# Kernel tuning notes

Hardware: AMD Instinct MI355X
Metric: run time of the kernel (lower is better)

Reference implementation:

```python
import jax, jax.numpy as jnp
import numpy as np

H = 16      # num_heads = num_channels // head_dim
D = 128     # head_dim
BLK = 64    # NABLA / flex_attention block size
THR = 0.8   # sparse_params['P'] cumulative-density threshold
EPS = 1e-6  # RMSNorm eps


def _rmsnorm(x, w):
    # torch nn.RMSNorm over last dim (computed in fp32 as in norm_qk)
    return x * jax.lax.rsqrt(jnp.mean(x * x, axis=-1, keepdims=True) + EPS) * w


def _rotate_half(x):
    x1, x2 = jnp.split(x, 2, axis=-1)
    return jnp.concatenate([-x2, x1], axis=-1)


def _apply_rotary(x, cos, sin):
    # x: [S, H, D]; cos/sin: [S, 1, D]
    return x * cos + _rotate_half(x) * sin


def _nabla_block_mask(q, k, sta_mask):
    # q, k: [H, S, D] -> block-pooled attention map, cumulative-density threshold
    Hh, S, Dd = q.shape
    nb = S // BLK
    qb = q.reshape(Hh, nb, BLK, Dd).mean(axis=2)           # [H, nQ, D]
    kb = k.reshape(Hh, nb, BLK, Dd).mean(axis=2)           # [H, nK, D]
    p = jax.nn.softmax(jnp.einsum('hqd,hkd->hqk', qb, kb) / np.sqrt(Dd), axis=-1)
    srt = -jnp.sort(-p, axis=-1)                           # descending
    csum = jnp.cumsum(srt, axis=-1)
    keep_sorted = (csum - srt) < THR                       # smallest set covering THR mass
    cutoff = jnp.min(jnp.where(keep_sorted, srt, jnp.inf), axis=-1, keepdims=True)
    return (p >= cutoff) | sta_mask[None]                  # [H, nQ, nK] bool


def reference(x, rope_cos, rope_sin, sta_mask, Wq, bq, Wk, bk, Wv, bv, Wo, bo, qn_w, kn_w):
    S, C = x.shape
    q = (x @ Wq + bq).reshape(S, H, D)
    k = (x @ Wk + bk).reshape(S, H, D)
    v = (x @ Wv + bv).reshape(S, H, D)
    q = _rmsnorm(q, qn_w)
    k = _rmsnorm(k, kn_w)
    q = _apply_rotary(q, rope_cos, rope_sin)
    k = _apply_rotary(k, rope_cos, rope_sin)
    q = q.transpose(1, 0, 2)  # [H, S, D]
    k = k.transpose(1, 0, 2)
    v = v.transpose(1, 0, 2)
    blk_keep = _nabla_block_mask(q, k, sta_mask)                     # [H, nQ, nK]
    mask = jnp.repeat(jnp.repeat(blk_keep, BLK, axis=1), BLK, axis=2)  # [H, S, S]
    scores = jnp.einsum('hqd,hkd->hqk', q, k) / np.sqrt(D)
    scores = jnp.where(mask, scores, -jnp.inf)
    attn = jax.nn.softmax(scores, axis=-1)
    out = jnp.einsum('hqk,hkd->hqd', attn, v)                        # [H, S, D]
    out = out.transpose(1, 0, 2).reshape(S, H * D)
    return out @ Wo + bo


def setup_inputs() -> dict:
    key = jax.random.key(0)
    ks = jax.random.split(key, 12)
    S, C = 2048, 2048
    nb = S // BLK
    sc = 0.02
    return {
        'x': jax.random.normal(ks[0], (S, C), jnp.float32),
        'rope_cos': jax.random.uniform(ks[1], (S, 1, D), jnp.float32),
        'rope_sin': jax.random.uniform(ks[2], (S, 1, D), jnp.float32),
        'sta_mask': jax.random.randint(ks[3], (nb, nb), 0, 2).astype(bool),
        'Wq': jax.random.normal(ks[4], (C, C), jnp.float32) * sc,
        'bq': jnp.zeros((C,), jnp.float32),
        'Wk': jax.random.normal(ks[5], (C, C), jnp.float32) * sc,
        'bk': jnp.zeros((C,), jnp.float32),
        'Wv': jax.random.normal(ks[6], (C, C), jnp.float32) * sc,
        'bv': jnp.zeros((C,), jnp.float32),
        'Wo': jax.random.normal(ks[7], (C, C), jnp.float32) * sc,
        'bo': jnp.zeros((C,), jnp.float32),
        'qn_w': jnp.ones((D,), jnp.float32),
        'kn_w': jnp.ones((D,), jnp.float32),
    }
```

## Files before the change

kernel.cpp:

```cpp
#include <hip/hip_runtime.h>


#define S_LEN 2048
#define CDIM  2048
#define NH    16
#define HD    128
#define NB    32

typedef __attribute__((ext_vector_type(8))) short s8v;
typedef __attribute__((ext_vector_type(4))) short s4v;
typedef __attribute__((ext_vector_type(4))) float f4v;

__device__ __forceinline__ short f2bf(float f){
  unsigned u = __builtin_bit_cast(unsigned, f);
  u += 0x7fffu + ((u>>16)&1u);
  return (short)(u>>16);
}
__device__ __forceinline__ float bf2f(short s){
  unsigned u = ((unsigned)(unsigned short)s)<<16;
  return __builtin_bit_cast(float, u);
}
__device__ __forceinline__ void gload_lds16(const void* g, void* l){
  __builtin_amdgcn_global_load_lds(
      (const __attribute__((address_space(1))) void*)g,
      (__attribute__((address_space(3))) void*)l, 16, 0, 0);
}

__global__ void __launch_bounds__(256) conv_x_kernel(
    const float* __restrict__ x, short* __restrict__ xcat)
{
  int i = blockIdx.x*256 + threadIdx.x;
  f4v v = ((const f4v*)x)[i];
  int s = i >> 9, c4 = (i & 511)*4;
  s4v hi, lo;
#pragma unroll
  for (int e=0;e<4;e++){
    short h = f2bf(v[e]);
    hi[e] = h;
    lo[e] = f2bf(v[e] - bf2f(h));
  }
  short* row = xcat + (size_t)s*4096 + c4;
  *(s4v*)(row)        = hi;
  *(s4v*)(row + 2048) = lo;
}

__global__ void __launch_bounds__(256) conv_w3_kernel(
    const float* __restrict__ W, short* __restrict__ wcat)
{
  __shared__ float tile[64][65];
  const int k0 = blockIdx.y*64, n0 = blockIdx.x*64, t = threadIdx.x;
#pragma unroll
  for (int i=0;i<16;i++){
    int idx = i*256 + t, r = idx>>6, c = idx&63;
    tile[r][c] = W[(size_t)(k0+r)*2048 + (n0+c)];
  }
  __syncthreads();
#pragma unroll
  for (int i=0;i<16;i++){
    int idx = i*256 + t, n = idx>>6, k = idx&63;
    float v = tile[k][n];
    short h  = f2bf(v);
    short lo = f2bf(v - bf2f(h));
    short* base = wcat + (size_t)(n0+n)*4096 + (k0+k);
    base[0]    = h;
    base[2048] = lo;
  }
}

__global__ void __launch_bounds__(256) conv_w1_kernel(
    const float* __restrict__ W, short* __restrict__ wt)
{
  __shared__ float tile[64][65];
  const int k0 = blockIdx.y*64, n0 = blockIdx.x*64, t = threadIdx.x;
#pragma unroll
  for (int i=0;i<16;i++){
    int idx = i*256 + t, r = idx>>6, c = idx&63;
    tile[r][c] = W[(size_t)(k0+r)*2048 + (n0+c)];
  }
  __syncthreads();
#pragma unroll
  for (int i=0;i<16;i++){
    int idx = i*256 + t, n = idx>>6, k = idx&63;
    wt[(size_t)(n0+n)*2048 + (k0+k)] = f2bf(tile[k][n]);
  }
}

__global__ void __launch_bounds__(512, 2) gemm_qk(
    const short* __restrict__ A,
    const short* __restrict__ Bt,
    const float* __restrict__ bq, const float* __restrict__ bk,
    float* __restrict__ Cout)
{
  __shared__ short Alds[2][256*64];
  __shared__ short Blds[2][128*64];
  const int t = threadIdx.x, w = t>>6, l = t&63;
  const int bid = blockIdx.x;
  const int swz = (bid & 7)*32 + (bid >> 3);
  const int m0 = (swz >> 5)*256, n0 = (swz & 31)*128;
  const int wr = w>>1, wc = w&1;
  const int l16 = l&15, lg = l>>4;

  f4v acc[4][4];
  f4v z = {0.f,0.f,0.f,0.f};
#pragma unroll
  for (int a=0;a<4;a++)
#pragma unroll
    for (int b=0;b<4;b++) acc[a][b] = z;

  const int srA = w*32 + (l>>3);
  const int srB = w*16 + (l>>3);
  const int scol = ((l&7) ^ ((l>>3)&7)) * 8;
  const short* Ag = A  + (size_t)(m0 + srA)*4096 + scol;
  const short* Bg = Bt + (size_t)(n0 + srB)*4096 + scol;

  auto stage = [&](int buf, int kt){
    const int ak = (kt < 2048) ? kt : kt - 2048;
    const int bk2 = (kt < 4096) ? kt : kt - 4096;
#pragma unroll
    for (int ii=0;ii<4;ii++)
      gload_lds16(Ag + (size_t)ii*8*4096 + ak, (char*)Alds[buf] + w*4096 + ii*1024);
#pragma unroll
    for (int ii=0;ii<2;ii++)
      gload_lds16(Bg + (size_t)ii*8*4096 + bk2, (char*)Blds[buf] + w*2048 + ii*1024);
  };

  stage(0, 0);
  int cur = 0;
  for (int kt = 0; kt < 6144; kt += 64){
    if (kt + 64 < 6144){
      stage(cur^1, kt+64);
      asm volatile("s_waitcnt vmcnt(6)" ::: "memory");
    } else {
      asm volatile("s_waitcnt vmcnt(0)" ::: "memory");
    }
    __builtin_amdgcn_s_barrier();
    const char* Al = (const char*)Alds[cur];
    const char* Bl = (const char*)Blds[cur];
#pragma unroll
    for (int kk=0;kk<2;kk++){
      const int swx = ((l16&7)<<4);
      const int koff = (kk*64 + lg*16);
      s8v af[4], bfv[4];
#pragma unroll
      for (int mt=0;mt<4;mt++)
        af[mt]  = *(const s8v*)(Al + (wr*64+mt*16+l16)*128 + (koff ^ swx));
#pragma unroll
      for (int nt=0;nt<4;nt++)
        bfv[nt] = *(const s8v*)(Bl + (wc*64+nt*16+l16)*128 + (koff ^ swx));
      __builtin_amdgcn_s_setprio(1);
#pragma unroll
      for (int mt=0;mt<4;mt++)
#pragma unroll
        for (int nt=0;nt<4;nt++)
          acc[mt][nt] = __builtin_amdgcn_mfma_f32_16x16x32_bf16(
              af[mt], bfv[nt], acc[mt][nt], 0, 0, 0);
      __builtin_amdgcn_s_setprio(0);
    }
    asm volatile("" ::: "memory");
    __builtin_amdgcn_s_barrier();
    cur ^= 1;
  }

  const float* bp = (n0 >= 2048) ? (bk + (n0 - 2048)) : (bq + n0);
#pragma unroll
  for (int mt=0;mt<4;mt++)
#pragma unroll
    for (int r=0;r<4;r++){
      int row = m0 + wr*64 + mt*16 + lg*4 + r;
#pragma unroll
      for (int nt=0;nt<4;nt++){
        int cr = wc*64 + nt*16 + l16;
        Cout[(size_t)row*4096 + n0 + cr] = acc[mt][nt][r] + bp[cr];
      }
    }
}

template<int OUT>
__global__ void __launch_bounds__(512, 4) gemm8_bt(
    const short* __restrict__ A, int lda,
    const short* __restrict__ Bt, int ldb,
    const float* __restrict__ bias,
    void* __restrict__ Cout, int ldc, int K, int ntiles)
{
  __shared__ short Alds[2][128*64];
  __shared__ short Blds[2][128*64];
  const int t = threadIdx.x, w = t>>6, l = t&63;
  const int nwg = gridDim.x;
  const int bid = blockIdx.x;
  const int swz = (bid & 7)*(nwg>>3) + (bid>>3);
  const int mi = swz / ntiles, ni = swz % ntiles;
  const int m0 = mi*128, n0 = ni*128;
  const int wr = w>>2, wc = w&3;
  const int l16 = l&15, lg = l>>4;

  f4v acc[4][2];
  f4v z = {0.f,0.f,0.f,0.f};
#pragma unroll
  for (int a=0;a<4;a++)
#pragma unroll
    for (int b=0;b<2;b++) acc[a][b] = z;

  const int srow = w*16 + (l>>3);
  const int scol = ((l&7) ^ ((l>>3)&7)) * 8;
  const short* Ag = A  + (size_t)(m0 + srow)*lda + scol;
  const short* Bg = Bt + (size_t)(n0 + srow)*ldb + scol;

  auto stageAB = [&](int buf, int kt){
#pragma unroll
    for (int ii=0;ii<2;ii++){
      gload_lds16(Ag + (size_t)ii*8*lda + kt, (char*)Alds[buf] + w*2048 + ii*1024);
      gload_lds16(Bg + (size_t)ii*8*ldb + kt, (char*)Blds[buf] + w*2048 + ii*1024);
    }
  };

  stageAB(0, 0);
  int cur = 0;
  for (int kt = 0; kt < K; kt += 64){
    if (kt + 64 < K){
      stageAB(cur^1, kt+64);
      asm volatile("s_waitcnt vmcnt(4)" ::: "memory");
    } else {
      asm volatile("s_waitcnt vmcnt(0)" ::: "memory");
    }
    __builtin_amdgcn_s_barrier();
    const char* Al = (const char*)Alds[cur];
    const char* Bl = (const char*)Blds[cur];
#pragma unroll
    for (int kk=0;kk<2;kk++){
      const int swx = ((l16&7)<<4);
      s8v af[4], bfv[2];
#pragma unroll
      for (int mt=0;mt<4;mt++)
        af[mt]  = *(const s8v*)(Al + (wr*64+mt*16+l16)*128 + ((kk*64 + lg*16) ^ swx));
#pragma unroll
      for (int jt=0;jt<2;jt++)
        bfv[jt] = *(const s8v*)(Bl + (wc*32+jt*16+l16)*128 + ((kk*64 + lg*16) ^ swx));
      __builtin_amdgcn_s_setprio(1);
#pragma unroll
      for (int mt=0;mt<4;mt++)
#pragma unroll
        for (int jt=0;jt<2;jt++)
          acc[mt][jt] = __builtin_amdgcn_mfma_f32_16x16x32_bf16(
              af[mt], bfv[jt], acc[mt][jt], 0, 0, 0);
      __builtin_amdgcn_s_setprio(0);
    }
    asm volatile("" ::: "memory");
    __builtin_amdgcn_s_barrier();
    cur ^= 1;
  }

#pragma unroll
  for (int mt=0;mt<4;mt++)
#pragma unroll
    for (int r=0;r<4;r++){
      int row = m0 + wr*64 + mt*16 + lg*4 + r;
#pragma unroll
      for (int jt=0;jt<2;jt++){
        int cr = wc*32 + jt*16 + l16;
        float v = acc[mt][jt][r] + bias[n0 + cr];
        if (OUT == 0) ((float*)Cout)[(size_t)row*ldc + n0 + cr] = v;
        else          ((short*)Cout)[(size_t)row*ldc + n0 + cr] = f2bf(v);
      }
    }
}

__global__ void __launch_bounds__(256) qk_post_kernel(
    const float* __restrict__ QKf,
    const float* __restrict__ qw, const float* __restrict__ kw,
    const float* __restrict__ rc, const float* __restrict__ rs,
    short* __restrict__ Qh, short* __restrict__ Kh,
    float* __restrict__ Qb, float* __restrict__ Kb)
{
  __shared__ float pool[4][128];
  const int sb = blockIdx.x, h = blockIdx.y, which = blockIdx.z;
  const float* in    = QKf + (which ? 2048 : 0);
  const float* wvp   = which ? kw : qw;
  short*       outp  = which ? Kh : Qh;
  float*       poolp = which ? Kb : Qb;
  const int t = threadIdx.x, w = t>>6, l = t&63;
  const int s = sb*64 + w*16 + (l>>2), d0 = (l&3)*32;

  float a[32];
  const f4v* src = (const f4v*)(in + (size_t)s*4096 + h*128 + d0);
#pragma unroll
  for (int i=0;i<8;i++){
    f4v v = src[i];
    a[i*4]=v[0]; a[i*4+1]=v[1]; a[i*4+2]=v[2]; a[i*4+3]=v[3];
  }
  float ss = 0.f;
#pragma unroll
  for (int i=0;i<32;i++) ss += a[i]*a[i];
  ss += __shfl_xor(ss,1); ss += __shfl_xor(ss,2);
  float rstd = 1.0f / sqrtf(ss*(1.0f/128.0f) + 1e-6f);

  const f4v* wv4 = (const f4v*)(wvp + d0);
#pragma unroll
  for (int i=0;i<8;i++){
    f4v wv = wv4[i];
    a[i*4]   *= rstd*wv[0]; a[i*4+1] *= rstd*wv[1];
    a[i*4+2] *= rstd*wv[2]; a[i*4+3] *= rstd*wv[3];
  }
  float cv[32], sv[32];
  const f4v* cs4 = (const f4v*)(rc + (size_t)s*128 + d0);
  const f4v* sn4 = (const f4v*)(rs + (size_t)s*128 + d0);
#pragma unroll
  for (int i=0;i<8;i++){
    f4v c = cs4[i], sn = sn4[i];
    cv[i*4]=c[0]; cv[i*4+1]=c[1]; cv[i*4+2]=c[2]; cv[i*4+3]=c[3];
    sv[i*4]=sn[0]; sv[i*4+1]=sn[1]; sv[i*4+2]=sn[2]; sv[i*4+3]=sn[3];
  }
  const float sgn = (l&2) ? 1.f : -1.f;
#pragma unroll
  for (int i=0;i<32;i++){
    float pv = __shfl_xor(a[i], 2);
    a[i] = a[i]*cv[i] + sgn*pv*sv[i];
  }
  short* op = outp + ((size_t)h*2048 + s)*128 + d0;
#pragma unroll
  for (int c8=0;c8<8;c8++){
    s4v ob;
#pragma unroll
    for (int e=0;e<4;e++) ob[e] = f2bf(a[c8*4+e]);
    ((s4v*)op)[c8] = ob;
  }
#pragma unroll
  for (int i=0;i<32;i++){
    a[i] += __shfl_xor(a[i],4);
    a[i] += __shfl_xor(a[i],8);
    a[i] += __shfl_xor(a[i],16);
    a[i] += __shfl_xor(a[i],32);
  }
  if ((l>>2)==0){
#pragma unroll
    for (int i=0;i<32;i++) pool[w][d0+i] = a[i];
  }
  __syncthreads();
  if (t < 128)
    poolp[((size_t)h*32 + sb)*128 + t] =
        (pool[0][t]+pool[1][t]+pool[2][t]+pool[3][t]) * (1.0f/64.0f);
}

__global__ void __launch_bounds__(64) nabla_mask_kernel(
    const float* __restrict__ Qb, const float* __restrict__ Kb,
    const void* __restrict__ sta, unsigned char* __restrict__ keep)
{
  const int qi = blockIdx.x, h = blockIdx.y, l = threadIdx.x;
  const int j = l & 31;
  const int* si = (const int*)sta;
  int wv0 = si[j];
  int isInt = __all((wv0==0) | (wv0==1));

  const f4v* qr = (const f4v*)(Qb + ((size_t)h*32+qi)*128);
  const f4v* kr = (const f4v*)(Kb + ((size_t)h*32+j)*128);
  float dot = 0.f;
#pragma unroll
  for (int d=0; d<32; d++){
    f4v a = qr[d], b = kr[d];
    dot += a[0]*b[0] + a[1]*b[1] + a[2]*b[2] + a[3]*b[3];
  }
  float logit = dot / sqrtf(128.0f);
  float mx = logit;
  mx = fmaxf(mx, __shfl_xor(mx,1));  mx = fmaxf(mx, __shfl_xor(mx,2));
  mx = fmaxf(mx, __shfl_xor(mx,4));  mx = fmaxf(mx, __shfl_xor(mx,8));
  mx = fmaxf(mx, __shfl_xor(mx,16));
  float e = expf(logit - mx);
  float den = e;
  den += __shfl_xor(den,1);  den += __shfl_xor(den,2);
  den += __shfl_xor(den,4);  den += __shfl_xor(den,8);
  den += __shfl_xor(den,16);
  float p = e / den;
  float Sg = 0.f;
  for (int jj=0;jj<32;jj++){
    float pj = __shfl(p, jj);
    if (pj > p) Sg += pj;
  }
  float cand = (Sg < 0.8f) ? p : 3.0e38f;
  float cut = cand;
  cut = fminf(cut, __shfl_xor(cut,1));  cut = fminf(cut, __shfl_xor(cut,2));
  cut = fminf(cut, __shfl_xor(cut,4));  cut = fminf(cut, __shfl_xor(cut,8));
  cut = fminf(cut, __shfl_xor(cut,16));
  bool stab = isInt ? (si[qi*32+j] != 0)
                    : (((const unsigned char*)sta)[qi*32+j] != 0);
  if (l < 32)
    keep[((size_t)(h*32)+qi)*32 + j] = ((p >= cut) || stab) ? 1 : 0;
}

__global__ void __launch_bounds__(256) v_trans_kernel(
    const short* __restrict__ v_sd, short* __restrict__ vt)
{
  __shared__ short tile[64][65];
  const int sb = blockIdx.x, db = blockIdx.y, h = blockIdx.z, t = threadIdx.x;
#pragma unroll
  for (int i=0;i<16;i++){
    int idx = i*256 + t, r = idx>>6, c = idx&63;
    tile[r][c] = v_sd[(size_t)(sb*64+r)*2048 + h*128 + db*64 + c];
  }
  __syncthreads();
#pragma unroll
  for (int i=0;i<16;i++){
    int idx = i*256 + t, dn = idx>>6, s2 = idx&63;
    vt[((size_t)h*128 + db*64 + dn)*2048 + sb*64 + s2] = tile[s2][dn];
  }
}

__global__ void __launch_bounds__(256) attn_fwd_kernel(
    const short* __restrict__ qh, const short* __restrict__ kh,
    const short* __restrict__ vt, const unsigned char* __restrict__ keep,
    short* __restrict__ attn_out)
{
  __shared__ short Klds[2][64*128];
  __shared__ short Vlds[2][128*64];
  __shared__ short Plds[4][1024];
  const int bid = blockIdx.x;
  const int swz = (bid & 7)*64 + (bid >> 3);
  const int h = swz >> 5, qb = swz & 31;
  const int t = threadIdx.x, w = t>>6, l = t&63;
  const int l16 = l&15, lg = l>>4;

  s8v qf[4];
  const int sq0 = qb*64 + w*16;
  const short* qbase = qh + ((size_t)h*2048 + sq0 + l16)*128 + lg*8;
#pragma unroll
  for (int kf=0;kf<4;kf++) qf[kf] = *(const s8v*)(qbase + kf*32);

  f4v acc[8];
  f4v z = {0.f,0.f,0.f,0.f};
#pragma unroll
  for (int d=0;d<8;d++) acc[d] = z;
  float mrow[4], lsum[4];
#pragma unroll
  for (int r=0;r<4;r++){ mrow[r] = -3.0e38f; lsum[r] = 0.f; }

  const unsigned char* keeprow = keep + ((size_t)(h*32) + qb)*32;
  const short* kg0 = kh + (size_t)h*2048*128;
  const short* vg0 = vt + (size_t)h*128*2048;

  unsigned km = 0;
#pragma unroll
  for (int j=0;j<32;j++) km |= ((unsigned)keeprow[j]) << j;
  if (!km) km = 1;

  auto stageKV = [&](int buf, int j){
    const char* kg = (const char*)(kg0 + (size_t)(j*64)*128);
    const char* vg = (const char*)(vg0 + j*64);
#pragma unroll
    for (int ii=0;ii<4;ii++){
      int kr = (w*4+ii)*4 + (l>>4);
      int ks = ((l&15)*16) ^ ((kr&7)<<4);
      gload_lds16(kg + (size_t)kr*256 + ks, (char*)Klds[buf] + (w*4+ii)*1024);
      int vr = (w*4+ii)*8 + (l>>3);
      int vs = ((l&7)*16) ^ ((vr&7)<<4);
      gload_lds16(vg + (size_t)vr*4096 + vs, (char*)Vlds[buf] + (w*4+ii)*1024);
    }
  };

  asm volatile("s_waitcnt vmcnt(0)" ::: "memory");
  int jcur = (int)__builtin_ctz(km); km &= km-1;
  stageKV(0, jcur);
  int cur = 0;

  while (jcur >= 0){
    int jn = -1;
    if (km){ jn = (int)__builtin_ctz(km); km &= km-1; }
    if (jn >= 0){
      stageKV(cur^1, jn);
      asm volatile("s_waitcnt vmcnt(8)" ::: "memory");
    } else {
      asm volatile("s_waitcnt vmcnt(0)" ::: "memory");
    }
    __builtin_amdgcn_s_barrier();

    const char* Kl = (const char*)Klds[cur];
    const char* Vl = (const char*)Vlds[cur];

    f4v sacc[4];
#pragma unroll
    for (int nt=0;nt<4;nt++) sacc[nt] = z;
    __builtin_amdgcn_s_setprio(1);
#pragma unroll
    for (int kf=0;kf<4;kf++)
#pragma unroll
      for (int nt=0;nt<4;nt++){
        int kr = nt*16 + l16;
        s8v bfr = *(const s8v*)(Kl + ((kr*256 + kf*64 + lg*16) ^ ((kr&7)<<4)));
        sacc[nt] = __builtin_amdgcn_mfma_f32_16x16x32_bf16(qf[kf], bfr, sacc[nt], 0,0,0);
      }
    __builtin_amdgcn_s_setprio(0);
    const float scl = 0.08838834764831845f;
#pragma unroll
    for (int nt=0;nt<4;nt++) sacc[nt] *= scl;

#pragma unroll
    for (int r=0;r<4;r++){
      float mx = fmaxf(fmaxf(sacc[0][r], sacc[1][r]),
                       fmaxf(sacc[2][r], sacc[3][r]));
      mx = fmaxf(mx, __shfl_xor(mx,1));  mx = fmaxf(mx, __shfl_xor(mx,2));
      mx = fmaxf(mx, __shfl_xor(mx,4));  mx = fmaxf(mx, __shfl_xor(mx,8));
      float mnew = fmaxf(mrow[r], mx);
      float resc = __expf(mrow[r] - mnew);
      mrow[r] = mnew;
      float psum = 0.f;
#pragma unroll
      for (int nt=0;nt<4;nt++){
        float p = __expf(sacc[nt][r] - mnew);
        sacc[nt][r] = p;
        psum += p;
      }
      psum += __shfl_xor(psum,1);  psum += __shfl_xor(psum,2);
      psum += __shfl_xor(psum,4);  psum += __shfl_xor(psum,8);
      lsum[r] = lsum[r]*resc + psum;
#pragma unroll
      for (int dt=0;dt<8;dt++) acc[dt][r] *= resc;
    }

    char* Pl = (char*)Plds[w];
#pragma unroll
    for (int nt=0;nt<4;nt++)
#pragma unroll
      for (int r=0;r<4;r++){
        int pr = lg*4 + r;
        *(short*)(Pl + ((pr*128 + nt*32 + l16*2) ^ ((pr&7)<<4))) = f2bf(sacc[nt][r]);
      }
    s8v pa0 = *(const s8v*)(Pl + ((l16*128 +  0 + lg*16) ^ ((l16&7)<<4)));
    s8v pa1 = *(const s8v*)(Pl + ((l16*128 + 64 + lg*16) ^ ((l16&7)<<4)));

    __builtin_amdgcn_s_setprio(1);
#pragma unroll
    for (int kk=0;kk<2;kk++){
      s8v pa = kk ? pa1 : pa0;
#pragma unroll
      for (int dt=0;dt<8;dt++){
        int vr = dt*16 + l16;
        s8v vb = *(const s8v*)(Vl + ((vr*128 + kk*64 + lg*16) ^ ((vr&7)<<4)));
        acc[dt] = __builtin_amdgcn_mfma_f32_16x16x32_bf16(pa, vb, acc[dt], 0,0,0);
      }
    }
    __builtin_amdgcn_s_setprio(0);

    asm volatile("" ::: "memory");
    __builtin_amdgcn_s_barrier();
    cur ^= 1; jcur = jn;
  }

#pragma unroll
  for (int r=0;r<4;r++){
    float inv = 1.0f / lsum[r];
    int s = qb*64 + w*16 + lg*4 + r;
#pragma unroll
    for (int dt=0;dt<8;dt++)
      attn_out[(size_t)s*2048 + h*128 + dt*16 + l16] = f2bf(acc[dt][r]*inv);
  }
}

extern "C" void kernel_launch(void* const* d_in, const int* in_sizes, int n_in,
                              void* d_out, int out_size, void* d_ws, size_t ws_size,
                              hipStream_t stream)
{
  (void)in_sizes; (void)n_in; (void)out_size; (void)ws_size;
  const float* x   = (const float*)d_in[0];
  const float* rc  = (const float*)d_in[1];
  const float* rs  = (const float*)d_in[2];
  const void*  sta = d_in[3];
  const float* Wq  = (const float*)d_in[4];
  const float* bq  = (const float*)d_in[5];
  const float* Wk  = (const float*)d_in[6];
  const float* bk  = (const float*)d_in[7];
  const float* Wv  = (const float*)d_in[8];
  const float* bv  = (const float*)d_in[9];
  const float* Wo  = (const float*)d_in[10];
  const float* bo  = (const float*)d_in[11];
  const float* qnw = (const float*)d_in[12];
  const float* knw = (const float*)d_in[13];

  char* ws = (char*)d_ws;
  size_t off = 0;
  auto take = [&](size_t b){ char* p = ws + off; off = (off + b + 255) & ~(size_t)255; return p; };
  short* Xcat  = (short*)take((size_t)2048*4096*2);
  short* Wcat2 = (short*)take((size_t)4096*4096*2);
  short* Wt1   = (short*)take((size_t)2048*2048*2);
  float* QKf   = (float*)take((size_t)2048*4096*4);
  short* Vsd   = (short*)take((size_t)2048*2048*2);
  short* Qh    = (short*)take((size_t)NH*2048*128*2);
  short* Kh    = (short*)take((size_t)NH*2048*128*2);
  float* Qb    = (float*)take((size_t)NH*32*128*4);
  float* Kb    = (float*)take((size_t)NH*32*128*4);
  unsigned char* Keep = (unsigned char*)take(NH*32*32);
  short* AttnO = (short*)QKf;
  short* Vt    = (short*)((char*)QKf + (size_t)16*1024*1024);

  conv_x_kernel <<<4096, 256, 0, stream>>>(x, Xcat);
  conv_w3_kernel<<<dim3(32,32), 256, 0, stream>>>(Wq, Wcat2);
  conv_w3_kernel<<<dim3(32,32), 256, 0, stream>>>(Wk, Wcat2 + (size_t)2048*4096);
  gemm_qk<<<256, 512, 0, stream>>>(Xcat, Wcat2, bq, bk, QKf);
  conv_w1_kernel<<<dim3(32,32), 256, 0, stream>>>(Wv, Wt1);
  gemm8_bt<1><<<256, 512, 0, stream>>>(Xcat, 4096, Wt1, 2048, bv, Vsd, 2048, 2048, 16);
  qk_post_kernel<<<dim3(32,16,2), 256, 0, stream>>>(QKf, qnw, knw, rc, rs, Qh, Kh, Qb, Kb);
  v_trans_kernel<<<dim3(32,2,16), 256, 0, stream>>>(Vsd, Vt);
  nabla_mask_kernel<<<dim3(32,16), 64, 0, stream>>>(Qb, Kb, sta, Keep);
  attn_fwd_kernel<<<512, 256, 0, stream>>>(Qh, Kh, Vt, Keep, AttnO);
  conv_w1_kernel<<<dim3(32,32), 256, 0, stream>>>(Wo, Wt1);
  gemm8_bt<0><<<256, 512, 0, stream>>>((const short*)AttnO, 2048, Wt1, 2048, bo, d_out, 2048, 2048, 16);
}
```

Before: 476.6 us.

## Retile projection GEMMs, batch weight conversions, and skip redundant softmax rescales

Drops the dedicated 256x128 QK GEMM and reuses the generic 128x128 kernel, extended with K-wrap offsets and a split bias, launched as 512 workgroups so the grid fills more CUs. A new 128x64-tile GEMM with higher occupancy handles the V and output projections, again with 512 workgroups. Weight conversion launches are merged using blockIdx.z, and Wo conversion moves out of the critical path behind attention. In attention, the online-softmax rescale now runs only when the row max grows, trading a branch for fewer multiplies. Smaller tiles lower data reuse per workgroup and raise total global traffic.

```diff
diff --git a/kernel.cpp b/kernel.cpp
--- a/kernel.cpp
+++ b/kernel.cpp
@@ -45,9 +45,12 @@
 }
 
 __global__ void __launch_bounds__(256) conv_w3_kernel(
-    const float* __restrict__ W, short* __restrict__ wcat)
+    const float* __restrict__ Wq, const float* __restrict__ Wk,
+    short* __restrict__ wcat)
 {
   __shared__ float tile[64][65];
+  const float* W = blockIdx.z ? Wk : Wq;
+  short* out = wcat + (size_t)blockIdx.z*2048*4096;
   const int k0 = blockIdx.y*64, n0 = blockIdx.x*64, t = threadIdx.x;
 #pragma unroll
   for (int i=0;i<16;i++){
@@ -61,16 +64,19 @@
     float v = tile[k][n];
     short h  = f2bf(v);
     short lo = f2bf(v - bf2f(h));
-    short* base = wcat + (size_t)(n0+n)*4096 + (k0+k);
+    short* base = out + (size_t)(n0+n)*4096 + (k0+k);
     base[0]    = h;
     base[2048] = lo;
   }
 }
 
 __global__ void __launch_bounds__(256) conv_w1_kernel(
-    const float* __restrict__ W, short* __restrict__ wt)
+    const float* __restrict__ Wv, const float* __restrict__ Wo,
+    short* __restrict__ wtv, short* __restrict__ wto)
 {
   __shared__ float tile[64][65];
+  const float* W = blockIdx.z ? Wo : Wv;
+  short* wt = blockIdx.z ? wto : wtv;
   const int k0 = blockIdx.y*64, n0 = blockIdx.x*64, t = threadIdx.x;
 #pragma unroll
   for (int i=0;i<16;i++){
@@ -83,104 +89,16 @@
     int idx = i*256 + t, n = idx>>6, k = idx&63;
     wt[(size_t)(n0+n)*2048 + (k0+k)] = f2bf(tile[k][n]);
   }
-}
-
-__global__ void __launch_bounds__(512, 2) gemm_qk(
-    const short* __restrict__ A,
-    const short* __restrict__ Bt,
-    const float* __restrict__ bq, const float* __restrict__ bk,
-    float* __restrict__ Cout)
-{
-  __shared__ short Alds[2][256*64];
-  __shared__ short Blds[2][128*64];
-  const int t = threadIdx.x, w = t>>6, l = t&63;
-  const int bid = blockIdx.x;
-  const int swz = (bid & 7)*32 + (bid >> 3);
-  const int m0 = (swz >> 5)*256, n0 = (swz & 31)*128;
-  const int wr = w>>1, wc = w&1;
-  const int l16 = l&15, lg = l>>4;
-
-  f4v acc[4][4];
-  f4v z = {0.f,0.f,0.f,0.f};
-#pragma unroll
-  for (int a=0;a<4;a++)
-#pragma unroll
-    for (int b=0;b<4;b++) acc[a][b] = z;
-
-  const int srA = w*32 + (l>>3);
-  const int srB = w*16 + (l>>3);
-  const int scol = ((l&7) ^ ((l>>3)&7)) * 8;
-  const short* Ag = A  + (size_t)(m0 + srA)*4096 + scol;
-  const short* Bg = Bt + (size_t)(n0 + srB)*4096 + scol;
-
-  auto stage = [&](int buf, int kt){
-    const int ak = (kt < 2048) ? kt : kt - 2048;
-    const int bk2 = (kt < 4096) ? kt : kt - 4096;
-#pragma unroll
-    for (int ii=0;ii<4;ii++)
-      gload_lds16(Ag + (size_t)ii*8*4096 + ak, (char*)Alds[buf] + w*4096 + ii*1024);
-#pragma unroll
-    for (int ii=0;ii<2;ii++)
-      gload_lds16(Bg + (size_t)ii*8*4096 + bk2, (char*)Blds[buf] + w*2048 + ii*1024);
-  };
-
-  stage(0, 0);
-  int cur = 0;
-  for (int kt = 0; kt < 6144; kt += 64){
-    if (kt + 64 < 6144){
-      stage(cur^1, kt+64);
-      asm volatile("s_waitcnt vmcnt(6)" ::: "memory");
-    } else {
-      asm volatile("s_waitcnt vmcnt(0)" ::: "memory");
-    }
-    __builtin_amdgcn_s_barrier();
-    const char* Al = (const char*)Alds[cur];
-    const char* Bl = (const char*)Blds[cur];
-#pragma unroll
-    for (int kk=0;kk<2;kk++){
-      const int swx = ((l16&7)<<4);
-      const int koff = (kk*64 + lg*16);
-      s8v af[4], bfv[4];
-#pragma unroll
-      for (int mt=0;mt<4;mt++)
-        af[mt]  = *(const s8v*)(Al + (wr*64+mt*16+l16)*128 + (koff ^ swx));
-#pragma unroll
-      for (int nt=0;nt<4;nt++)
-        bfv[nt] = *(const s8v*)(Bl + (wc*64+nt*16+l16)*128 + (koff ^ swx));
-      __builtin_amdgcn_s_setprio(1);
-#pragma unroll
-      for (int mt=0;mt<4;mt++)
-#pragma unroll
-        for (int nt=0;nt<4;nt++)
-          acc[mt][nt] = __builtin_amdgcn_mfma_f32_16x16x32_bf16(
-              af[mt], bfv[nt], acc[mt][nt], 0, 0, 0);
-      __builtin_amdgcn_s_setprio(0);
-    }
-    asm volatile("" ::: "memory");
-    __builtin_amdgcn_s_barrier();
-    cur ^= 1;
-  }
-
-  const float* bp = (n0 >= 2048) ? (bk + (n0 - 2048)) : (bq + n0);
-#pragma unroll
-  for (int mt=0;mt<4;mt++)
-#pragma unroll
-    for (int r=0;r<4;r++){
-      int row = m0 + wr*64 + mt*16 + lg*4 + r;
-#pragma unroll
-      for (int nt=0;nt<4;nt++){
-        int cr = wc*64 + nt*16 + l16;
-        Cout[(size_t)row*4096 + n0 + cr] = acc[mt][nt][r] + bp[cr];
-      }
-    }
 }
 
 template<int OUT>
 __global__ void __launch_bounds__(512, 4) gemm8_bt(
     const short* __restrict__ A, int lda,
     const short* __restrict__ Bt, int ldb,
-    const float* __restrict__ bias,
-    void* __restrict__ Cout, int ldc, int K, int ntiles)
+    const float* __restrict__ biasQ, const float* __restrict__ biasK,
+    int nsplit,
+    void* __restrict__ Cout, int ldc, int K, int ntiles,
+    int awrap, int asub, int bwrap, int bsub)
 {
   __shared__ short Alds[2][128*64];
   __shared__ short Blds[2][128*64];
@@ -206,10 +124,12 @@
   const short* Bg = Bt + (size_t)(n0 + srow)*ldb + scol;
 
   auto stageAB = [&](int buf, int kt){
+    const int ak = kt - ((kt >= awrap) ? asub : 0);
+    const int bk2 = kt - ((kt >= bwrap) ? bsub : 0);
 #pragma unroll
     for (int ii=0;ii<2;ii++){
-      gload_lds16(Ag + (size_t)ii*8*lda + kt, (char*)Alds[buf] + w*2048 + ii*1024);
-      gload_lds16(Bg + (size_t)ii*8*ldb + kt, (char*)Blds[buf] + w*2048 + ii*1024);
+      gload_lds16(Ag + (size_t)ii*8*lda + ak, (char*)Alds[buf] + w*2048 + ii*1024);
+      gload_lds16(Bg + (size_t)ii*8*ldb + bk2, (char*)Blds[buf] + w*2048 + ii*1024);
     }
   };
 
@@ -249,6 +169,7 @@
     cur ^= 1;
   }
 
+  const float* bp = (n0 >= nsplit) ? (biasK + (n0 - nsplit)) : (biasQ + n0);
 #pragma unroll
   for (int mt=0;mt<4;mt++)
 #pragma unroll
@@ -257,10 +178,89 @@
 #pragma unroll
       for (int jt=0;jt<2;jt++){
         int cr = wc*32 + jt*16 + l16;
-        float v = acc[mt][jt][r] + bias[n0 + cr];
+        float v = acc[mt][jt][r] + bp[cr];
         if (OUT == 0) ((float*)Cout)[(size_t)row*ldc + n0 + cr] = v;
         else          ((short*)Cout)[(size_t)row*ldc + n0 + cr] = f2bf(v);
       }
+    }
+}
+
+template<int OUT>
+__global__ void __launch_bounds__(512, 6) gemm8_n64(
+    const short* __restrict__ A, int lda,
+    const short* __restrict__ Bt, int ldb,
+    const float* __restrict__ bias,
+    void* __restrict__ Cout, int ldc, int K, int ntiles)
+{
+  __shared__ short Alds[2][128*64];
+  __shared__ short Blds[2][64*64];
+  const int t = threadIdx.x, w = t>>6, l = t&63;
+  const int nwg = gridDim.x;
+  const int bid = blockIdx.x;
+  const int swz = (bid & 7)*(nwg>>3) + (bid>>3);
+  const int mi = swz / ntiles, ni = swz % ntiles;
+  const int m0 = mi*128, n0 = ni*64;
+  const int wr = w>>2, wc = w&3;
+  const int l16 = l&15, lg = l>>4;
+
+  f4v acc[4];
+  f4v z = {0.f,0.f,0.f,0.f};
+#pragma unroll
+  for (int a=0;a<4;a++) acc[a] = z;
+
+  const int srA = w*16 + (l>>3);
+  const int srB = w*8  + (l>>3);
+  const int scol = ((l&7) ^ ((l>>3)&7)) * 8;
+  const short* Ag = A  + (size_t)(m0 + srA)*lda + scol;
+  const short* Bg = Bt + (size_t)(n0 + srB)*ldb + scol;
+
+  auto stageAB = [&](int buf, int kt){
+#pragma unroll
+    for (int ii=0;ii<2;ii++)
+      gload_lds16(Ag + (size_t)ii*8*lda + kt, (char*)Alds[buf] + w*2048 + ii*1024);
+    gload_lds16(Bg + kt, (char*)Blds[buf] + w*1024);
+  };
+
+  stageAB(0, 0);
+  int cur = 0;
+  for (int kt = 0; kt < K; kt += 64){
+    if (kt + 64 < K){
+      stageAB(cur^1, kt+64);
+      asm volatile("s_waitcnt vmcnt(3)" ::: "memory");
+    } else {
+      asm volatile("s_waitcnt vmcnt(0)" ::: "memory");
+    }
+    __builtin_amdgcn_s_barrier();
+    const char* Al = (const char*)Alds[cur];
+    const char* Bl = (const char*)Blds[cur];
+#pragma unroll
+    for (int kk=0;kk<2;kk++){
+      const int swx = ((l16&7)<<4);
+      s8v af[4], bfv;
+#pragma unroll
+      for (int mt=0;mt<4;mt++)
+        af[mt] = *(const s8v*)(Al + (wr*64+mt*16+l16)*128 + ((kk*64 + lg*16) ^ swx));
+      bfv = *(const s8v*)(Bl + (wc*16+l16)*128 + ((kk*64 + lg*16) ^ swx));
+      __builtin_amdgcn_s_setprio(1);
+#pragma unroll
+      for (int mt=0;mt<4;mt++)
+        acc[mt] = __builtin_amdgcn_mfma_f32_16x16x32_bf16(af[mt], bfv, acc[mt], 0,0,0);
+      __builtin_amdgcn_s_setprio(0);
+    }
+    asm volatile("" ::: "memory");
+    __builtin_amdgcn_s_barrier();
+    cur ^= 1;
+  }
+
+#pragma unroll
+  for (int mt=0;mt<4;mt++)
+#pragma unroll
+    for (int r=0;r<4;r++){
+      int row = m0 + wr*64 + mt*16 + lg*4 + r;
+      int cr = wc*16 + l16;
+      float v = acc[mt][r] + bias[n0 + cr];
+      if (OUT == 0) ((float*)Cout)[(size_t)row*ldc + n0 + cr] = v;
+      else          ((short*)Cout)[(size_t)row*ldc + n0 + cr] = f2bf(v);
     }
 }
 
@@ -496,21 +496,23 @@
                        fmaxf(sacc[2][r], sacc[3][r]));
       mx = fmaxf(mx, __shfl_xor(mx,1));  mx = fmaxf(mx, __shfl_xor(mx,2));
       mx = fmaxf(mx, __shfl_xor(mx,4));  mx = fmaxf(mx, __shfl_xor(mx,8));
-      float mnew = fmaxf(mrow[r], mx);
-      float resc = __expf(mrow[r] - mnew);
-      mrow[r] = mnew;
+      if (mx > mrow[r]){
+        float resc = __expf(mrow[r] - mx);
+        mrow[r] = mx;
+        lsum[r] *= resc;
+#pragma unroll
+        for (int dt=0;dt<8;dt++) acc[dt][r] *= resc;
+      }
       float psum = 0.f;
 #pragma unroll
       for (int nt=0;nt<4;nt++){
-        float p = __expf(sacc[nt][r] - mnew);
+        float p = __expf(sacc[nt][r] - mrow[r]);
         sacc[nt][r] = p;
         psum += p;
       }
       psum += __shfl_xor(psum,1);  psum += __shfl_xor(psum,2);
       psum += __shfl_xor(psum,4);  psum += __shfl_xor(psum,8);
-      lsum[r] = lsum[r]*resc + psum;
-#pragma unroll
-      for (int dt=0;dt<8;dt++) acc[dt][r] *= resc;
+      lsum[r] += psum;
     }
 
     char* Pl = (char*)Plds[w];
@@ -577,7 +579,8 @@
   auto take = [&](size_t b){ char* p = ws + off; off = (off + b + 255) & ~(size_t)255; return p; };
   short* Xcat  = (short*)take((size_t)2048*4096*2);
   short* Wcat2 = (short*)take((size_t)4096*4096*2);
-  short* Wt1   = (short*)take((size_t)2048*2048*2);
+  short* Wt1v  = (short*)take((size_t)2048*2048*2);
+  short* Wt1o  = (short*)take((size_t)2048*2048*2);
   float* QKf   = (float*)take((size_t)2048*4096*4);
   short* Vsd   = (short*)take((size_t)2048*2048*2);
   short* Qh    = (short*)take((size_t)NH*2048*128*2);
@@ -589,15 +592,17 @@
   short* Vt    = (short*)((char*)QKf + (size_t)16*1024*1024);
 
   conv_x_kernel <<<4096, 256, 0, stream>>>(x, Xcat);
-  conv_w3_kernel<<<dim3(32,32), 256, 0, stream>>>(Wq, Wcat2);
-  conv_w3_kernel<<<dim3(32,32), 256, 0, stream>>>(Wk, Wcat2 + (size_t)2048*4096);
-  gemm_qk<<<256, 512, 0, stream>>>(Xcat, Wcat2, bq, bk, QKf);
-  conv_w1_kernel<<<dim3(32,32), 256, 0, stream>>>(Wv, Wt1);
-  gemm8_bt<1><<<256, 512, 0, stream>>>(Xcat, 4096, Wt1, 2048, bv, Vsd, 2048, 2048, 16);
+  conv_w3_kernel<<<dim3(32,32,2), 256, 0, stream>>>(Wq, Wk, Wcat2);
+  gemm8_bt<0><<<512, 512, 0, stream>>>(Xcat, 4096, Wcat2, 4096, bq, bk, 2048,
+                                       QKf, 4096, 6144, 32,
+                                       2048, 2048, 4096, 4096);
+  conv_w1_kernel<<<dim3(32,32,2), 256, 0, stream>>>(Wv, Wo, Wt1v, Wt1o);
+  gemm8_n64<1><<<512, 512, 0, stream>>>(Xcat, 4096, Wt1v, 2048, bv,
+                                        Vsd, 2048, 2048, 32);
   qk_post_kernel<<<dim3(32,16,2), 256, 0, stream>>>(QKf, qnw, knw, rc, rs, Qh, Kh, Qb, Kb);
   v_trans_kernel<<<dim3(32,2,16), 256, 0, stream>>>(Vsd, Vt);
   nabla_mask_kernel<<<dim3(32,16), 64, 0, stream>>>(Qb, Kb, sta, Keep);
   attn_fwd_kernel<<<512, 256, 0, stream>>>(Qh, Kh, Vt, Keep, AttnO);
-  conv_w1_kernel<<<dim3(32,32), 256, 0, stream>>>(Wo, Wt1);
-  gemm8_bt<0><<<256, 512, 0, stream>>>((const short*)AttnO, 2048, Wt1, 2048, bo, d_out, 2048, 2048, 16);
-}
+  gemm8_n64<0><<<512, 512, 0, stream>>>((const short*)AttnO, 2048, Wt1o, 2048, bo,
+                                        d_out, 2048, 2048, 32);
+}
```

New measurement: 513.2 us. 7.7% more time.
